# Kernel tuning notes

Hardware: AMD Instinct MI355X
Metric: run time of the kernel (lower is better)

## Reference

```python
import jax, jax.numpy as jnp
import numpy as np

B, S, H, NH, L, FF, V, T = 16, 256, 768, 12, 12, 3072, 30522, 9
DH = H // NH
LN_EPS = 1e-12


def _ln(x, g, b):
    m = jnp.mean(x, axis=-1, keepdims=True)
    v = jnp.mean((x - m) ** 2, axis=-1, keepdims=True)
    return (x - m) * jax.lax.rsqrt(v + LN_EPS) * g + b


def setup_inputs():
    key = jax.random.key(0)
    ks = jax.random.split(key, 20)
    n = lambda i, shape: jax.random.normal(ks[i], shape, jnp.float32) * 0.02
    lengths = jax.random.randint(ks[0], (B,), S // 2, S + 1)
    attention_mask = (jnp.arange(S)[None, :] < lengths[:, None]).astype(jnp.int32)
    return {
        "input_ids": jax.random.randint(ks[1], (B, S), 0, V),
        "attention_mask": attention_mask,
        "labels": jax.random.randint(ks[2], (B, S), 0, T),
        "word_emb": n(3, (V, H)),
        "pos_emb": n(4, (512, H)),
        "type_emb": n(5, (2, H)),
        "emb_g": jnp.ones((H,), jnp.float32), "emb_b": jnp.zeros((H,), jnp.float32),
        "lWq": n(6, (L, H, H)), "lbq": jnp.zeros((L, H), jnp.float32),
        "lWk": n(7, (L, H, H)), "lbk": jnp.zeros((L, H), jnp.float32),
        "lWv": n(8, (L, H, H)), "lbv": jnp.zeros((L, H), jnp.float32),
        "lWo": n(9, (L, H, H)), "lbo": jnp.zeros((L, H), jnp.float32),
        "lg1": jnp.ones((L, H), jnp.float32), "lb1": jnp.zeros((L, H), jnp.float32),
        "lWi": n(10, (L, H, FF)), "lbi": jnp.zeros((L, FF), jnp.float32),
        "lWf": n(11, (L, FF, H)), "lbf": jnp.zeros((L, H), jnp.float32),
        "lg2": jnp.ones((L, H), jnp.float32), "lb2": jnp.zeros((L, H), jnp.float32),
        "cls_W": n(12, (H, T)), "cls_b": jnp.zeros((T,), jnp.float32),
        "crf_start": jax.random.uniform(ks[13], (T,), jnp.float32, -0.1, 0.1),
        "crf_end": jax.random.uniform(ks[14], (T,), jnp.float32, -0.1, 0.1),
        "crf_trans": jax.random.uniform(ks[15], (T, T), jnp.float32, -0.1, 0.1),
    }


def _encoder(input_ids, attention_mask, word_emb, pos_emb, type_emb, emb_g, emb_b, layer_stack, cls_W, cls_b):
    x = word_emb[input_ids] + pos_emb[:S][None] + type_emb[0][None, None]  # [B,S,H]
    x = _ln(x, emb_g, emb_b)
    bias = (1.0 - attention_mask.astype(jnp.float32))[:, None, None, :] * -1e9  # [B,1,1,S]
    scale = 1.0 / np.sqrt(DH).astype(np.float32)

    def layer(h, p):
        Wq, bq, Wk, bk, Wv, bv, Wo, bo, g1, b1, Wi, bi, Wf, bf, g2, b2 = p
        q = (h @ Wq + bq).reshape(B, S, NH, DH)
        k = (h @ Wk + bk).reshape(B, S, NH, DH)
        v = (h @ Wv + bv).reshape(B, S, NH, DH)
        att = jax.nn.softmax(jnp.einsum('bqhd,bkhd->bhqk', q, k) * scale + bias, axis=-1)
        ctx = jnp.einsum('bhqk,bkhd->bqhd', att, v).reshape(B, S, H)
        h = _ln(h + ctx @ Wo + bo, g1, b1)
        ff = jax.nn.gelu(h @ Wi + bi, approximate=False) @ Wf + bf
        h = _ln(h + ff, g2, b2)
        return h, None

    x, _ = jax.lax.scan(layer, x, layer_stack)
    return x @ cls_W + cls_b  # [B,S,T]


def _crf_llh(em, tg, m, start, end, trans):
    # pytorch-crf forward, reduction='sum'. em [B,Lc,T], tg [B,Lc] int, m [B,Lc] bool
    mf = m.astype(em.dtype)
    em_sc = jnp.take_along_axis(em, tg[..., None], axis=-1)[..., 0]  # [B,Lc]
    tr_sc = trans[tg[:, :-1], tg[:, 1:]]                             # [B,Lc-1]
    num = start[tg[:, 0]] + em_sc[:, 0] + jnp.sum(mf[:, 1:] * (tr_sc + em_sc[:, 1:]), axis=1)
    seq_ends = jnp.sum(m.astype(jnp.int32), axis=1) - 1
    last_tag = jnp.take_along_axis(tg, seq_ends[:, None], axis=1)[:, 0]
    num = num + end[last_tag]

    def step(score, xs):
        em_t, m_t = xs
        nxt = jax.nn.logsumexp(score[:, :, None] + trans[None] + em_t[:, None, :], axis=1)
        return jnp.where(m_t[:, None], nxt, score), None

    score0 = start[None] + em[:, 0]
    score, _ = jax.lax.scan(step, score0, (em[:, 1:].transpose(1, 0, 2), m[:, 1:].transpose(1, 0)))
    den = jax.nn.logsumexp(score + end[None], axis=1)
    return jnp.sum(num - den)


def _viterbi(em, start, end, trans):
    # decode over the FULL sequence with all-ones mask (matches crf.decode(logits))
    def step(score, em_t):
        cand = score[:, :, None] + trans[None] + em_t[:, None, :]  # [B,T,T]
        return jnp.max(cand, axis=1), jnp.argmax(cand, axis=1)

    score0 = start[None] + em[:, 0]
    score, hist = jax.lax.scan(step, score0, em[:, 1:].transpose(1, 0, 2))  # hist [S-1,B,T]
    last = jnp.argmax(score + end[None], axis=1)  # [B]

    def back(tag, h):
        prev = jnp.take_along_axis(h, tag[:, None], axis=1)[:, 0]
        return prev, prev

    _, rev = jax.lax.scan(back, last, hist, reverse=True)  # rev[i] = tag at time i, i in [0,S-2]
    tags = jnp.concatenate([rev.transpose(1, 0), last[:, None]], axis=1)  # [B,S]
    return tags.astype(jnp.float32)


def reference(input_ids, attention_mask, labels, word_emb, pos_emb, type_emb, emb_g, emb_b,
              lWq, lbq, lWk, lbk, lWv, lbv, lWo, lbo, lg1, lb1, lWi, lbi, lWf, lbf, lg2, lb2,
              cls_W, cls_b, crf_start, crf_end, crf_trans):
    layer_stack = (lWq, lbq, lWk, lbk, lWv, lbv, lWo, lbo, lg1, lb1, lWi, lbi, lWf, lbf, lg2, lb2)
    logits = _encoder(input_ids, attention_mask, word_emb, pos_emb, type_emb, emb_g, emb_b, layer_stack, cls_W, cls_b)
    str_lens = jnp.sum(attention_mask, axis=-1)
    pos = jnp.arange(S)[None, :]
    mask = attention_mask.astype(bool) & (pos > 0) & (pos != (str_lens - 1)[:, None])
    tags_in = jnp.where(mask, labels, jnp.zeros_like(labels))
    loss = -_crf_llh(logits[:, 1:], tags_in[:, 1:], mask[:, 1:], crf_start, crf_end, crf_trans)
    tags = _viterbi(logits, crf_start, crf_end, crf_trans)
    return (loss, tags)
```

## Files before the change

### kernel.cpp

```cpp
#include <hip/hip_runtime.h>

#define B_ 16
#define S_ 256
#define H_ 768
#define NH_ 12
#define DH_ 64
#define L_ 12
#define FF_ 3072
#define T_ 9
#define NTOK (B_*S_)

#define AS1 __attribute__((address_space(1)))
#define AS3 __attribute__((address_space(3)))

typedef __attribute__((ext_vector_type(8))) short bfrag;
typedef __attribute__((ext_vector_type(8))) unsigned short us8;
typedef __attribute__((ext_vector_type(4))) float f4;

#define LOG2E_ 1.4426950408889634f
#define LN2_   0.6931471805599453f

__device__ inline unsigned short f2bf(float x) {
    unsigned u = __builtin_bit_cast(unsigned, x);
    return (unsigned short)((u + 0x7fffu + ((u >> 16) & 1u)) >> 16);
}
__device__ inline float bf2f(unsigned short h) {
    unsigned u = ((unsigned)h) << 16;
    return __builtin_bit_cast(float, u);
}
__device__ inline void pack8(const float* v, us8& h, us8& l) {
    #pragma unroll
    for (int j = 0; j < 8; j++) {
        unsigned short hh = f2bf(v[j]);
        h[j] = hh;
        l[j] = f2bf(v[j] - bf2f(hh));
    }
}

__global__ __launch_bounds__(256) void k_conv_w(
    const float* __restrict__ Wq, const float* __restrict__ Wk,
    const float* __restrict__ Wv, const float* __restrict__ Wo,
    const float* __restrict__ Wi, const float* __restrict__ Wf,
    const float* __restrict__ bq, const float* __restrict__ bk, const float* __restrict__ bv,
    float* __restrict__ qkvbias, unsigned short* __restrict__ Wpk)
{
    int bid = blockIdx.x;
    int tid = threadIdx.x;
    if (bid == 0) {
        for (int i = tid; i < 3 * H_; i += 256)
            qkvbias[i] = (i < H_) ? bq[i] : (i < 2 * H_) ? bk[i - H_] : bv[i - 2 * H_];
    }
    const float* src; int Kd, Nd; size_t doff; int t;
    if (bid < 576)       { int m = bid / 144; src = (m == 0) ? Wq : (m == 1) ? Wk : (m == 2) ? Wv : Wo;
                           Kd = H_; Nd = H_; doff = (size_t)m * 73728; t = bid % 144; }
    else if (bid < 1152) { src = Wi; Kd = H_; Nd = FF_; doff = 294912; t = bid - 576; }
    else                 { src = Wf; Kd = FF_; Nd = H_; doff = 589824; t = bid - 1152; }
    int ntn = Nd / 64;
    int tk = t / ntn, tn = t % ntn;
    int k0 = tk * 64, n0 = tn * 64;
    __shared__ float tile[64][65];
    int r = tid >> 6, c = tid & 63;
    #pragma unroll
    for (int i = 0; i < 16; i++)
        tile[r + i * 4][c] = src[(size_t)(k0 + r + i * 4) * Nd + n0 + c];
    __syncthreads();
    #pragma unroll
    for (int e = 0; e < 2; e++) {
        int item = tid * 2 + e;
        int nl = item >> 3, kb = item & 7;
        float v8[8];
        #pragma unroll
        for (int j = 0; j < 8; j++) v8[j] = tile[kb * 8 + j][nl];
        us8 h, l; pack8(v8, h, l);
        unsigned short* p = Wpk + (doff + (size_t)(n0 + nl) * (Kd / 8) + (k0 / 8 + kb)) * 16;
        *reinterpret_cast<us8*>(p) = h;
        *reinterpret_cast<us8*>(p + 8) = l;
    }
}

__global__ __launch_bounds__(128) void k_embed_ln(
    const int* __restrict__ ids, const float* __restrict__ wemb,
    const float* __restrict__ pemb, const float* __restrict__ temb,
    const float* __restrict__ g, const float* __restrict__ bb,
    float* __restrict__ out, unsigned short* __restrict__ out_pk)
{
    int tok = blockIdx.x;
    int s = tok & (S_ - 1);
    int id = ids[tok];
    int tid = threadIdx.x;
    bool act = tid < 96;
    int idx = tid * 8;
    float v8[8];
    float sum = 0.f;
    if (act) {
        const float4* w4 = reinterpret_cast<const float4*>(wemb + (size_t)id * H_ + idx);
        const float4* p4 = reinterpret_cast<const float4*>(pemb + (size_t)s * H_ + idx);
        const float4* t4 = reinterpret_cast<const float4*>(temb + idx);
        #pragma unroll
        for (int q = 0; q < 2; q++) {
            float4 a = w4[q], b = p4[q], c = t4[q];
            v8[q*4+0] = a.x + b.x + c.x; v8[q*4+1] = a.y + b.y + c.y;
            v8[q*4+2] = a.z + b.z + c.z; v8[q*4+3] = a.w + b.w + c.w;
        }
        #pragma unroll
        for (int j = 0; j < 8; j++) sum += v8[j];
    }
    __shared__ float wsum[2], wvar[2];
    #pragma unroll
    for (int o = 32; o > 0; o >>= 1) sum += __shfl_xor(sum, o);
    if ((tid & 63) == 0) wsum[tid >> 6] = sum;
    __syncthreads();
    float mean = (wsum[0] + wsum[1]) * (1.0f / H_);
    float vs = 0.f;
    if (act) {
        for (int j = 0; j < 8; j++) { float d = v8[j] - mean; vs += d * d; }
    }
    #pragma unroll
    for (int o = 32; o > 0; o >>= 1) vs += __shfl_xor(vs, o);
    if ((tid & 63) == 0) wvar[tid >> 6] = vs;
    __syncthreads();
    float inv = 1.0f / sqrtf((wvar[0] + wvar[1]) * (1.0f / H_) + 1e-12f);
    if (act) {
        float o8[8];
        #pragma unroll
        for (int j = 0; j < 8; j++) o8[j] = (v8[j] - mean) * inv * g[idx + j] + bb[idx + j];
        float4* d4 = reinterpret_cast<float4*>(out + (size_t)tok * H_ + idx);
        d4[0] = make_float4(o8[0], o8[1], o8[2], o8[3]);
        d4[1] = make_float4(o8[4], o8[5], o8[6], o8[7]);
        us8 h, l; pack8(o8, h, l);
        unsigned short* p = out_pk + ((size_t)tok * 96 + tid) * 16;
        *reinterpret_cast<us8*>(p) = h;
        *reinterpret_cast<us8*>(p + 8) = l;
    }
}

__global__ __launch_bounds__(128) void k_res_ln(
    const float* __restrict__ x, const float* __restrict__ res,
    const float* __restrict__ g, const float* __restrict__ bb,
    float* __restrict__ out, unsigned short* __restrict__ out_pk)
{
    int tok = blockIdx.x;
    int tid = threadIdx.x;
    bool act = tid < 96;
    int idx = tid * 8;
    float v8[8];
    float sum = 0.f;
    if (act) {
        const float4* x4 = reinterpret_cast<const float4*>(x + (size_t)tok * H_ + idx);
        const float4* r4 = reinterpret_cast<const float4*>(res + (size_t)tok * H_ + idx);
        #pragma unroll
        for (int q = 0; q < 2; q++) {
            float4 a = x4[q], b = r4[q];
            v8[q*4+0] = a.x + b.x; v8[q*4+1] = a.y + b.y;
            v8[q*4+2] = a.z + b.z; v8[q*4+3] = a.w + b.w;
        }
        #pragma unroll
        for (int j = 0; j < 8; j++) sum += v8[j];
    }
    __shared__ float wsum[2], wvar[2];
    #pragma unroll
    for (int o = 32; o > 0; o >>= 1) sum += __shfl_xor(sum, o);
    if ((tid & 63) == 0) wsum[tid >> 6] = sum;
    __syncthreads();
    float mean = (wsum[0] + wsum[1]) * (1.0f / H_);
    float vs = 0.f;
    if (act) {
        for (int j = 0; j < 8; j++) { float d = v8[j] - mean; vs += d * d; }
    }
    #pragma unroll
    for (int o = 32; o > 0; o >>= 1) vs += __shfl_xor(vs, o);
    if ((tid & 63) == 0) wvar[tid >> 6] = vs;
    __syncthreads();
    float inv = 1.0f / sqrtf((wvar[0] + wvar[1]) * (1.0f / H_) + 1e-12f);
    if (act) {
        float o8[8];
        #pragma unroll
        for (int j = 0; j < 8; j++) o8[j] = (v8[j] - mean) * inv * g[idx + j] + bb[idx + j];
        float4* d4 = reinterpret_cast<float4*>(out + (size_t)tok * H_ + idx);
        d4[0] = make_float4(o8[0], o8[1], o8[2], o8[3]);
        d4[1] = make_float4(o8[4], o8[5], o8[6], o8[7]);
        us8 h, l; pack8(o8, h, l);
        unsigned short* p = out_pk + ((size_t)tok * 96 + tid) * 16;
        *reinterpret_cast<us8*>(p) = h;
        *reinterpret_cast<us8*>(p + 8) = l;
    }
}

__global__ __launch_bounds__(256) void k_gemm_pk(
    const unsigned short* __restrict__ A, const unsigned short* __restrict__ Wp,
    const float* __restrict__ bias,
    float* __restrict__ C0, float* __restrict__ C1, float* __restrict__ C2, int cpb,
    unsigned short* __restrict__ Cpk,
    int M, int N, int K, int act, int cbx)
{
    constexpr int BUFSZ = 24576;
    __shared__ char smem[3 * BUFSZ];
    unsigned smb = (unsigned)(size_t)(void*)smem;

    int id = blockIdx.x;
    int xcd = id & 7;
    int rr = id >> 3;
    int by = (xcd >> 1) * 8 + rr / cbx;
    int bx = (xcd & 1) * cbx + rr % cbx;
    int m0 = by << 7, n0 = bx << 6;
    int Kb = K >> 3;
    int nst = Kb >> 2;
    int rowbytes = Kb * 32;

    int tid = threadIdx.x;
    int lane = tid & 63, wid = tid >> 6;
    int wm = wid >> 1, wn = wid & 1;
    int fr = lane & 15, fq = lane >> 4;

    f4 acc[4][2];
    #pragma unroll
    for (int i = 0; i < 4; i++)
        #pragma unroll
        for (int j = 0; j < 2; j++) acc[i][j] = (f4){0.f, 0.f, 0.f, 0.f};

    const char* agp[4];
    const char* bgp[2];
    #pragma unroll
    for (int i = 0; i < 4; i++) {
        int d = i * 4096 + tid * 16;
        int row = d >> 7;
        int colp = (d & 127) ^ ((row & 7) << 4);
        agp[i] = (const char*)A + (size_t)(m0 + row) * rowbytes + colp;
    }
    #pragma unroll
    for (int i = 0; i < 2; i++) {
        int d = i * 4096 + tid * 16;
        int row = d >> 7;
        int colp = (d & 127) ^ ((row & 7) << 4);
        bgp[i] = (const char*)Wp + (size_t)(n0 + row) * rowbytes + colp;
    }

    int afo[4], bfo[2];
    #pragma unroll
    for (int mi = 0; mi < 4; mi++) {
        int r = wm * 64 + mi * 16 + fr;
        afo[mi] = r * 128 + ((fq * 32) ^ ((r & 7) << 4));
    }
    #pragma unroll
    for (int ni = 0; ni < 2; ni++) {
        int rb = wn * 32 + ni * 16 + fr;
        bfo[ni] = 16384 + rb * 128 + ((fq * 32) ^ ((rb & 7) << 4));
    }

    auto issue = [&](int ks, unsigned boff) {
        size_t ko = (size_t)ks * 128;
        #pragma unroll
        for (int i = 0; i < 4; i++)
            __builtin_amdgcn_global_load_lds((const AS1 void*)(size_t)(agp[i] + ko),
                (AS3 void*)(unsigned)(smb + boff + i * 4096 + wid * 1024), 16, 0, 0);
        #pragma unroll
        for (int i = 0; i < 2; i++)
            __builtin_amdgcn_global_load_lds((const AS1 void*)(size_t)(bgp[i] + ko),
                (AS3 void*)(unsigned)(smb + boff + 16384 + i * 4096 + wid * 1024), 16, 0, 0);
    };

    issue(0, 0);
    if (nst > 1) issue(1, BUFSZ);
    unsigned c0 = 0, c1 = BUFSZ, c2 = 2 * BUFSZ;

    for (int ks = 0; ks < nst; ks++) {
        if (ks + 2 < nst) issue(ks + 2, c2);
        if (ks + 2 < nst)      asm volatile("s_waitcnt vmcnt(12)" ::: "memory");
        else if (ks + 1 < nst) asm volatile("s_waitcnt vmcnt(6)" ::: "memory");
        else                   asm volatile("s_waitcnt vmcnt(0)" ::: "memory");
        __builtin_amdgcn_s_barrier();
        __builtin_amdgcn_sched_barrier(0);

        const char* cbp = smem + c0;
        bfrag ah[4], al[4], bh[2], bl[2];
        #pragma unroll
        for (int mi = 0; mi < 4; mi++) {
            ah[mi] = *reinterpret_cast<const bfrag*>(cbp + afo[mi]);
            al[mi] = *reinterpret_cast<const bfrag*>(cbp + (afo[mi] ^ 16));
        }
        #pragma unroll
        for (int ni = 0; ni < 2; ni++) {
            bh[ni] = *reinterpret_cast<const bfrag*>(cbp + bfo[ni]);
            bl[ni] = *reinterpret_cast<const bfrag*>(cbp + (bfo[ni] ^ 16));
        }
        #pragma unroll
        for (int mi = 0; mi < 4; mi++) {
            #pragma unroll
            for (int ni = 0; ni < 2; ni++) {
                acc[mi][ni] = __builtin_amdgcn_mfma_f32_16x16x32_bf16(ah[mi], bh[ni], acc[mi][ni], 0, 0, 0);
                acc[mi][ni] = __builtin_amdgcn_mfma_f32_16x16x32_bf16(ah[mi], bl[ni], acc[mi][ni], 0, 0, 0);
                acc[mi][ni] = __builtin_amdgcn_mfma_f32_16x16x32_bf16(al[mi], bh[ni], acc[mi][ni], 0, 0, 0);
            }
        }
        __builtin_amdgcn_s_barrier();
        __builtin_amdgcn_sched_barrier(0);
        unsigned t = c0; c0 = c1; c1 = c2; c2 = t;
    }

    if (act == 0) {
        #pragma unroll
        for (int mi = 0; mi < 4; mi++) {
            #pragma unroll
            for (int ni = 0; ni < 2; ni++) {
                int col = n0 + wn * 32 + ni * 16 + fr;
                float bv = bias[col];
                int buf = col / cpb;
                float* Cp = (buf == 0) ? C0 : (buf == 1) ? C1 : C2;
                int cc = col - buf * cpb;
                #pragma unroll
                for (int r = 0; r < 4; r++) {
                    int row = m0 + wm * 64 + mi * 16 + fq * 4 + r;
                    Cp[(size_t)row * cpb + cc] = acc[mi][ni][r] + bv;
                }
            }
        }
    } else {
        float* ebuf = (float*)(smem + wid * 2432);
        int Nb = N >> 3;
        #pragma unroll
        for (int mi = 0; mi < 4; mi++) {
            #pragma unroll
            for (int ni = 0; ni < 2; ni++) {
                int col = n0 + wn * 32 + ni * 16 + fr;
                float bv = bias[col];
                #pragma unroll
                for (int r = 0; r < 4; r++) {
                    float v = acc[mi][ni][r] + bv;
                    v = 0.5f * v * (1.0f + erff(v * 0.70710678118654752f));
                    ebuf[(fq * 4 + r) * 38 + ni * 16 + fr] = v;
                }
            }
            int row16 = lane >> 2, kb = lane & 3;
            float v8[8];
            #pragma unroll
            for (int j = 0; j < 8; j++) v8[j] = ebuf[row16 * 38 + kb * 8 + j];
            us8 h, l; pack8(v8, h, l);
            int grow = m0 + wm * 64 + mi * 16 + row16;
            int gcb = ((n0 + wn * 32) >> 3) + kb;
            unsigned short* p = Cpk + ((size_t)grow * Nb + gcb) * 16;
            *reinterpret_cast<us8*>(p) = h;
            *reinterpret_cast<us8*>(p + 8) = l;
        }
    }
}

#define SM_KH 0
#define SM_KL 5632
#define SM_VH 11264
#define SM_VL 16384
#define SM_PH 21504
#define SM_PL 26624
__global__ __launch_bounds__(256) void k_attn_fused(
    const float* __restrict__ Q, const float* __restrict__ Kb,
    const float* __restrict__ V, const int* __restrict__ amask,
    unsigned short* __restrict__ ctx_pk)
{
    __shared__ char smem[31744];
    unsigned short* KhS = (unsigned short*)(smem + SM_KH);
    unsigned short* KlS = (unsigned short*)(smem + SM_KL);
    unsigned short* VhS = (unsigned short*)(smem + SM_VH);
    unsigned short* VlS = (unsigned short*)(smem + SM_VL);
    unsigned short* PhS = (unsigned short*)(smem + SM_PH);
    unsigned short* PlS = (unsigned short*)(smem + SM_PL);

    int idx = blockIdx.x;
    int qt = idx & 3;
    int hd = (idx >> 2) % NH_;
    int b = idx / (4 * NH_);
    int tid = threadIdx.x;
    int lane = tid & 63, wid = tid >> 6;
    int fr = lane & 15, fq = lane >> 4;

    int q0 = qt * 64 + wid * 16;

    bfrag qh[2], ql[2];
    {
        const float* qbase = Q + ((size_t)(b * S_ + q0 + fr)) * H_ + hd * DH_;
        #pragma unroll
        for (int ks = 0; ks < 2; ks++) {
            const float4* p = reinterpret_cast<const float4*>(qbase + ks * 32 + fq * 8);
            float4 v0 = p[0], v1 = p[1];
            float vv[8] = {v0.x, v0.y, v0.z, v0.w, v1.x, v1.y, v1.z, v1.w};
            #pragma unroll
            for (int j = 0; j < 8; j++) {
                unsigned short h = f2bf(vv[j]);
                qh[ks][j] = (short)h;
                ql[ks][j] = (short)f2bf(vv[j] - bf2f(h));
            }
        }
    }

    f4 o[4];
    #pragma unroll
    for (int i = 0; i < 4; i++) o[i] = (f4){0.f, 0.f, 0.f, 0.f};
    float m[4], l[4];
    #pragma unroll
    for (int r = 0; r < 4; r++) { m[r] = -3e38f; l[r] = 0.f; }

    int kvrow = tid >> 3;
    int dbase = (tid & 7) * 8;

    for (int t = 0; t < 8; t++) {
        {
            const float* src = Kb + ((size_t)(b * S_ + t * 32 + kvrow)) * H_ + hd * DH_ + dbase;
            float4 a4 = reinterpret_cast<const float4*>(src)[0];
            float4 b4 = reinterpret_cast<const float4*>(src)[1];
            float vv[8] = {a4.x, a4.y, a4.z, a4.w, b4.x, b4.y, b4.z, b4.w};
            us8 h, l2;
            #pragma unroll
            for (int j = 0; j < 8; j++) {
                unsigned short hh = f2bf(vv[j]);
                h[j] = hh; l2[j] = f2bf(vv[j] - bf2f(hh));
            }
            *reinterpret_cast<us8*>(&KhS[kvrow * 88 + dbase]) = h;
            *reinterpret_cast<us8*>(&KlS[kvrow * 88 + dbase]) = l2;
        }
        {
            const float* src = V + ((size_t)(b * S_ + t * 32 + kvrow)) * H_ + hd * DH_ + dbase;
            float4 a4 = reinterpret_cast<const float4*>(src)[0];
            float4 b4 = reinterpret_cast<const float4*>(src)[1];
            float vv[8] = {a4.x, a4.y, a4.z, a4.w, b4.x, b4.y, b4.z, b4.w};
            #pragma unroll
            for (int j = 0; j < 8; j++) {
                unsigned short h = f2bf(vv[j]);
                VhS[(dbase + j) * 40 + kvrow] = h;
                VlS[(dbase + j) * 40 + kvrow] = f2bf(vv[j] - bf2f(h));
            }
        }
        __syncthreads();

        f4 s0 = (f4){0.f,0.f,0.f,0.f}, s1 = (f4){0.f,0.f,0.f,0.f};
        #pragma unroll
        for (int ks = 0; ks < 2; ks++) {
            bfrag kbh0 = *reinterpret_cast<const bfrag*>(&KhS[fr * 88 + ks * 32 + fq * 8]);
            bfrag kbl0 = *reinterpret_cast<const bfrag*>(&KlS[fr * 88 + ks * 32 + fq * 8]);
            bfrag kbh1 = *reinterpret_cast<const bfrag*>(&KhS[(16 + fr) * 88 + ks * 32 + fq * 8]);
            bfrag kbl1 = *reinterpret_cast<const bfrag*>(&KlS[(16 + fr) * 88 + ks * 32 + fq * 8]);
            s0 = __builtin_amdgcn_mfma_f32_16x16x32_bf16(qh[ks], kbh0, s0, 0, 0, 0);
            s0 = __builtin_amdgcn_mfma_f32_16x16x32_bf16(qh[ks], kbl0, s0, 0, 0, 0);
            s0 = __builtin_amdgcn_mfma_f32_16x16x32_bf16(ql[ks], kbh0, s0, 0, 0, 0);
            s1 = __builtin_amdgcn_mfma_f32_16x16x32_bf16(qh[ks], kbh1, s1, 0, 0, 0);
            s1 = __builtin_amdgcn_mfma_f32_16x16x32_bf16(qh[ks], kbl1, s1, 0, 0, 0);
            s1 = __builtin_amdgcn_mfma_f32_16x16x32_bf16(ql[ks], kbh1, s1, 0, 0, 0);
        }

        float cb0 = (amask[b * S_ + t * 32 + fr] == 0) ? -1e9f : 0.f;
        float cb1 = (amask[b * S_ + t * 32 + 16 + fr] == 0) ? -1e9f : 0.f;
        float sc0[4], sc1[4], fct[4], pr0[4], pr1[4];
        #pragma unroll
        for (int r = 0; r < 4; r++) {
            sc0[r] = s0[r] * 0.125f + cb0;
            sc1[r] = s1[r] * 0.125f + cb1;
            float tm = fmaxf(sc0[r], sc1[r]);
            #pragma unroll
            for (int od = 1; od < 16; od <<= 1) tm = fmaxf(tm, __shfl_xor(tm, od));
            float mn = fmaxf(m[r], tm);
            fct[r] = expf(m[r] - mn);
            pr0[r] = expf(sc0[r] - mn);
            pr1[r] = expf(sc1[r] - mn);
            float rs = pr0[r] + pr1[r];
            #pragma unroll
            for (int od = 1; od < 16; od <<= 1) rs += __shfl_xor(rs, od);
            l[r] = l[r] * fct[r] + rs;
            m[r] = mn;
        }
        #pragma unroll
        for (int ci = 0; ci < 4; ci++)
            #pragma unroll
            for (int r = 0; r < 4; r++) o[ci][r] *= fct[r];

        #pragma unroll
        for (int r = 0; r < 4; r++) {
            int row = fq * 4 + r;
            unsigned short h0 = f2bf(pr0[r]);
            PhS[wid * 640 + row * 40 + fr] = h0;
            PlS[wid * 640 + row * 40 + fr] = f2bf(pr0[r] - bf2f(h0));
            unsigned short h1 = f2bf(pr1[r]);
            PhS[wid * 640 + row * 40 + 16 + fr] = h1;
            PlS[wid * 640 + row * 40 + 16 + fr] = f2bf(pr1[r] - bf2f(h1));
        }

        bfrag pah = *reinterpret_cast<const bfrag*>(&PhS[wid * 640 + fr * 40 + fq * 8]);
        bfrag pal = *reinterpret_cast<const bfrag*>(&PlS[wid * 640 + fr * 40 + fq * 8]);
        #pragma unroll
        for (int ci = 0; ci < 4; ci++) {
            bfrag vbh = *reinterpret_cast<const bfrag*>(&VhS[(ci * 16 + fr) * 40 + fq * 8]);
            bfrag vbl = *reinterpret_cast<const bfrag*>(&VlS[(ci * 16 + fr) * 40 + fq * 8]);
            o[ci] = __builtin_amdgcn_mfma_f32_16x16x32_bf16(pah, vbh, o[ci], 0, 0, 0);
            o[ci] = __builtin_amdgcn_mfma_f32_16x16x32_bf16(pah, vbl, o[ci], 0, 0, 0);
            o[ci] = __builtin_amdgcn_mfma_f32_16x16x32_bf16(pal, vbh, o[ci], 0, 0, 0);
        }
        __syncthreads();
    }

    __syncthreads();
    float* eb = (float*)smem + wid * 1088;
    #pragma unroll
    for (int r = 0; r < 4; r++) {
        float inv = 1.0f / l[r];
        #pragma unroll
        for (int ci = 0; ci < 4; ci++)
            eb[(fq * 4 + r) * 68 + ci * 16 + fr] = o[ci][r] * inv;
    }
    __syncthreads();
    #pragma unroll
    for (int e = 0; e < 2; e++) {
        int item = lane * 2 + e;
        int row16 = item >> 3, kb = item & 7;
        float v8[8];
        #pragma unroll
        for (int j = 0; j < 8; j++) v8[j] = eb[row16 * 68 + kb * 8 + j];
        us8 h, l2; pack8(v8, h, l2);
        int grow = b * S_ + q0 + row16;
        int gcb = hd * 8 + kb;
        unsigned short* p = ctx_pk + ((size_t)grow * 96 + gcb) * 16;
        *reinterpret_cast<us8*>(p) = h;
        *reinterpret_cast<us8*>(p + 8) = l2;
    }
}

__global__ __launch_bounds__(64) void k_classifier(
    const float* __restrict__ Hs, const float* __restrict__ Wc,
    const float* __restrict__ bc, float* __restrict__ logits)
{
    int tok = blockIdx.x;
    int lane = threadIdx.x;
    const float* hr = Hs + (size_t)tok * H_;
    float acc[T_];
    #pragma unroll
    for (int j = 0; j < T_; j++) acc[j] = 0.f;
    for (int k = lane; k < H_; k += 64) {
        float hv = hr[k];
        const float* wr = Wc + (size_t)k * T_;
        #pragma unroll
        for (int j = 0; j < T_; j++) acc[j] = fmaf(hv, wr[j], acc[j]);
    }
    #pragma unroll
    for (int j = 0; j < T_; j++) {
        float v = acc[j];
        for (int o = 32; o > 0; o >>= 1) v += __shfl_down(v, o);
        if (lane == 0) logits[(size_t)tok * T_ + j] = v + bc[j];
    }
}

__global__ __launch_bounds__(256) void k_crf_vit(
    const float* __restrict__ logits, const int* __restrict__ amask,
    const int* __restrict__ labels, const float* __restrict__ start,
    const float* __restrict__ endv, const float* __restrict__ trans,
    float* __restrict__ out)
{
    int blk = blockIdx.x;
    int tid = threadIdx.x;
    if (blk == 0) {
        __shared__ float res[B_];
        int lane = tid & 63;
        int bb = (tid >> 6) * 4 + (lane >> 4);
        int sj = lane & 15;
        int lb = lane & 48;

        int cnt = 0;
        for (int s = sj; s < S_; s += 16) cnt += amask[bb * S_ + s];
        #pragma unroll
        for (int o = 8; o > 0; o >>= 1) cnt += __shfl_xor(cnt, o);
        int len = cnt;
        int lim = len - 1;

        float num = 0.f;
        for (int s = 2 + sj; s < S_; s += 16) {
            if (s < lim) {
                int tp = labels[bb * S_ + s - 1];
                int tc = labels[bb * S_ + s];
                num += trans[tp * T_ + tc] + logits[((size_t)(bb * S_ + s)) * T_ + tc];
            }
        }
        #pragma unroll
        for (int o = 8; o > 0; o >>= 1) num += __shfl_xor(num, o);
        int tg1 = labels[bb * S_ + 1];
        num += start[tg1] + logits[((size_t)(bb * S_ + 1)) * T_ + tg1];
        num += endv[labels[bb * S_ + (len - 2)]];

        float tc9[T_];
        #pragma unroll
        for (int i = 0; i < T_; i++) tc9[i] = (sj < T_) ? trans[i * T_ + sj] * LOG2E_ : 0.f;
        float score = (sj < T_) ? (start[sj] + logits[((size_t)(bb * S_ + 1)) * T_ + sj]) * LOG2E_ : 0.f;
        const float* embase = logits + (size_t)bb * S_ * T_ + sj;
        float emb[8];
        #pragma unroll
        for (int c = 0; c < 8; c++) emb[c] = (sj < T_) ? embase[(2 + c) * T_] : 0.f;
        for (int s0 = 2; s0 < S_; s0 += 8) {
            #pragma unroll
            for (int c = 0; c < 8; c++) {
                int s = s0 + c;
                if (s < S_) {
                    float em = emb[c];
                    emb[c] = (sj < T_ && s + 8 < S_) ? embase[(size_t)(s + 8) * T_] : 0.f;
                    float si[T_];
                    #pragma unroll
                    for (int i = 0; i < T_; i++) si[i] = __shfl(score, lb + i);
                    float a9[T_];
                    #pragma unroll
                    for (int i = 0; i < T_; i++) a9[i] = si[i] + tc9[i];
                    float mx = a9[0];
                    #pragma unroll
                    for (int i = 1; i < T_; i++) mx = fmaxf(mx, a9[i]);
                    float sum = 0.f;
                    #pragma unroll
                    for (int i = 0; i < T_; i++) sum += exp2f(a9[i] - mx);
                    float nsc = fmaf(em, LOG2E_, mx + log2f(sum));
                    if (s < lim) score = nsc;
                }
            }
        }
        float se = (sj < T_) ? score + endv[sj] * LOG2E_ : -1e30f;
        float fi[T_];
        #pragma unroll
        for (int i = 0; i < T_; i++) fi[i] = __shfl(se, lb + i);
        if (sj == 0) {
            float mx = -1e30f;
            #pragma unroll
            for (int i = 0; i < T_; i++) mx = fmaxf(mx, fi[i]);
            float sum = 0.f;
            #pragma unroll
            for (int i = 0; i < T_; i++) sum += exp2f(fi[i] - mx);
            res[bb] = (mx + log2f(sum)) * LN2_ - num;
        }
        __syncthreads();
        if (tid == 0) {
            float tot = 0.f;
            #pragma unroll
            for (int i = 0; i < B_; i++) tot += res[i];
            out[0] = tot;
        }
    } else {
        if (tid >= 64) return;
        int b = blk - 1;
        int j = tid;
        float* tags_out = out + 1;
        __shared__ unsigned char hist[S_ - 1][T_];
        float tc9[T_];
        #pragma unroll
        for (int i = 0; i < T_; i++) tc9[i] = (j < T_) ? trans[i * T_ + j] : 0.f;
        float score = (j < T_) ? start[j] + logits[((size_t)(b * S_)) * T_ + j] : -1e30f;
        const float* embase = logits + (size_t)b * S_ * T_ + j;
        float emb[8];
        #pragma unroll
        for (int c = 0; c < 8; c++) emb[c] = (j < T_) ? embase[(1 + c) * T_] : 0.f;
        for (int t0 = 1; t0 < S_; t0 += 8) {
            #pragma unroll
            for (int c = 0; c < 8; c++) {
                int t = t0 + c;
                if (t < S_) {
                    float em = emb[c];
                    emb[c] = (j < T_ && t + 8 < S_) ? embase[(size_t)(t + 8) * T_] : 0.f;
                    float si[T_];
                    #pragma unroll
                    for (int i = 0; i < T_; i++) si[i] = __shfl(score, i);
                    float best = -1e30f; int bi = 0;
                    #pragma unroll
                    for (int i = 0; i < T_; i++) {
                        float cv = si[i] + tc9[i];
                        if (cv > best) { best = cv; bi = i; }
                    }
                    if (j < T_) {
                        hist[t - 1][j] = (unsigned char)bi;
                        score = best + em;
                    }
                }
            }
        }
        float se = (j < T_) ? score + endv[j] : -1e30f;
        float fi[T_];
        #pragma unroll
        for (int i = 0; i < T_; i++) fi[i] = __shfl(se, i);
        if (j == 0) {
            float best = -1e30f; int last = 0;
            #pragma unroll
            for (int i = 0; i < T_; i++) if (fi[i] > best) { best = fi[i]; last = i; }
            tags_out[b * S_ + (S_ - 1)] = (float)last;
            int cur = last;
            for (int t = S_ - 2; t >= 0; t--) {
                cur = hist[t][cur];
                tags_out[b * S_ + t] = (float)cur;
            }
        }
    }
}

extern "C" void kernel_launch(void* const* d_in, const int* in_sizes, int n_in,
                              void* d_out, int out_size, void* d_ws, size_t ws_size,
                              hipStream_t stream)
{
    const int*   input_ids = (const int*)d_in[0];
    const int*   amask     = (const int*)d_in[1];
    const int*   labels    = (const int*)d_in[2];
    const float* word_emb  = (const float*)d_in[3];
    const float* pos_emb   = (const float*)d_in[4];
    const float* type_emb  = (const float*)d_in[5];
    const float* emb_g     = (const float*)d_in[6];
    const float* emb_b     = (const float*)d_in[7];
    const float* lWq = (const float*)d_in[8];
    const float* lbq = (const float*)d_in[9];
    const float* lWk = (const float*)d_in[10];
    const float* lbk = (const float*)d_in[11];
    const float* lWv = (const float*)d_in[12];
    const float* lbv = (const float*)d_in[13];
    const float* lWo = (const float*)d_in[14];
    const float* lbo = (const float*)d_in[15];
    const float* lg1 = (const float*)d_in[16];
    const float* lb1 = (const float*)d_in[17];
    const float* lWi = (const float*)d_in[18];
    const float* lbi = (const float*)d_in[19];
    const float* lWf = (const float*)d_in[20];
    const float* lbf = (const float*)d_in[21];
    const float* lg2 = (const float*)d_in[22];
    const float* lb2 = (const float*)d_in[23];
    const float* cls_W = (const float*)d_in[24];
    const float* cls_b = (const float*)d_in[25];
    const float* crf_start = (const float*)d_in[26];
    const float* crf_end   = (const float*)d_in[27];
    const float* crf_trans = (const float*)d_in[28];

    float* out = (float*)d_out;
    float* ws = (float*)d_ws;

    const size_t NH32 = (size_t)NTOK * H_;
    float* h       = ws;
    float* h_pk_f  = ws + NH32;
    float* q       = ws + 2 * NH32;
    float* kbuf    = ws + 3 * NH32;
    float* v       = ws + 4 * NH32;
    float* ctxpk_f = ws + 5 * NH32;
    float* tmp     = ws + 6 * NH32;
    float* Wpk_f   = ws + 7 * NH32;
    float* qkvbias = Wpk_f + 7077888;
    float* logits  = qkvbias + 3 * H_;

    unsigned short* h_pk   = (unsigned short*)h_pk_f;
    unsigned short* ctx_pk = (unsigned short*)ctxpk_f;
    unsigned short* Wpk    = (unsigned short*)Wpk_f;
    unsigned short* big_pk = (unsigned short*)q;

    k_embed_ln<<<NTOK, 128, 0, stream>>>(input_ids, word_emb, pos_emb, type_emb, emb_g, emb_b, h, h_pk);

    const size_t WOFF_O = 221184, WOFF_I = 294912, WOFF_F = 589824;

    for (int l = 0; l < L_; l++) {
        k_conv_w<<<1728, 256, 0, stream>>>(
            lWq + (size_t)l * H_ * H_, lWk + (size_t)l * H_ * H_,
            lWv + (size_t)l * H_ * H_, lWo + (size_t)l * H_ * H_,
            lWi + (size_t)l * H_ * FF_, lWf + (size_t)l * FF_ * H_,
            lbq + (size_t)l * H_, lbk + (size_t)l * H_, lbv + (size_t)l * H_,
            qkvbias, Wpk);

        k_gemm_pk<<<1152, 256, 0, stream>>>(h_pk, Wpk, qkvbias,
            q, kbuf, v, H_, nullptr, NTOK, 3 * H_, H_, 0, 18);

        k_attn_fused<<<B_ * NH_ * 4, 256, 0, stream>>>(q, kbuf, v, amask, ctx_pk);

        k_gemm_pk<<<384, 256, 0, stream>>>(ctx_pk, Wpk + WOFF_O * 16, lbo + (size_t)l * H_,
            tmp, tmp, tmp, H_, nullptr, NTOK, H_, H_, 0, 6);

        k_res_ln<<<NTOK, 128, 0, stream>>>(tmp, h, lg1 + (size_t)l * H_, lb1 + (size_t)l * H_, h, h_pk);

        k_gemm_pk<<<1536, 256, 0, stream>>>(h_pk, Wpk + WOFF_I * 16, lbi + (size_t)l * FF_,
            tmp, tmp, tmp, FF_, big_pk, NTOK, FF_, H_, 1, 24);

        k_gemm_pk<<<384, 256, 0, stream>>>(big_pk, Wpk + WOFF_F * 16, lbf + (size_t)l * H_,
            tmp, tmp, tmp, H_, nullptr, NTOK, H_, FF_, 0, 6);

        k_res_ln<<<NTOK, 128, 0, stream>>>(tmp, h, lg2 + (size_t)l * H_, lb2 + (size_t)l * H_, h, h_pk);
    }

    k_classifier<<<NTOK, 64, 0, stream>>>(h, cls_W, cls_b, logits);
    k_crf_vit<<<1 + B_, 256, 0, stream>>>(logits, amask, labels, crf_start, crf_end, crf_trans, out);
}
```

Measured before the change: 3.608 ms.

## Drop fp32 hidden copy, reorder GEMM prefetch barrier, simplify CRF reductions

The fp32 hidden-state buffer is removed. Residual adds and the classifier now rebuild activations from the packed bf16 hi/lo pair, which cuts global traffic in the LayerNorm and classifier kernels. The GEMM main loop issues the next-stage prefetch after the barrier and drops the second per-iteration barrier, adding a syncthreads before the epilogue. The CRF forward pass swaps max-subtraction for periodic rebasing of the score, and Viterbi uses a tree argmax. These changes risk small precision differences, and the triple-buffer ordering may race if the buffer reuse distance is off.

```diff
diff --git a/kernel.cpp b/kernel.cpp
--- a/kernel.cpp
+++ b/kernel.cpp
@@ -82,7 +82,7 @@
     const int* __restrict__ ids, const float* __restrict__ wemb,
     const float* __restrict__ pemb, const float* __restrict__ temb,
     const float* __restrict__ g, const float* __restrict__ bb,
-    float* __restrict__ out, unsigned short* __restrict__ out_pk)
+    unsigned short* __restrict__ out_pk)
 {
     int tok = blockIdx.x;
     int s = tok & (S_ - 1);
@@ -124,9 +124,6 @@
         float o8[8];
         #pragma unroll
         for (int j = 0; j < 8; j++) o8[j] = (v8[j] - mean) * inv * g[idx + j] + bb[idx + j];
-        float4* d4 = reinterpret_cast<float4*>(out + (size_t)tok * H_ + idx);
-        d4[0] = make_float4(o8[0], o8[1], o8[2], o8[3]);
-        d4[1] = make_float4(o8[4], o8[5], o8[6], o8[7]);
         us8 h, l; pack8(o8, h, l);
         unsigned short* p = out_pk + ((size_t)tok * 96 + tid) * 16;
         *reinterpret_cast<us8*>(p) = h;
@@ -135,9 +132,8 @@
 }
 
 __global__ __launch_bounds__(128) void k_res_ln(
-    const float* __restrict__ x, const float* __restrict__ res,
-    const float* __restrict__ g, const float* __restrict__ bb,
-    float* __restrict__ out, unsigned short* __restrict__ out_pk)
+    const float* __restrict__ x, const float* __restrict__ g, const float* __restrict__ bb,
+    unsigned short* __restrict__ h_pk)
 {
     int tok = blockIdx.x;
     int tid = threadIdx.x;
@@ -145,17 +141,18 @@
     int idx = tid * 8;
     float v8[8];
     float sum = 0.f;
+    unsigned short* p = h_pk + ((size_t)tok * 96 + tid) * 16;
     if (act) {
         const float4* x4 = reinterpret_cast<const float4*>(x + (size_t)tok * H_ + idx);
-        const float4* r4 = reinterpret_cast<const float4*>(res + (size_t)tok * H_ + idx);
-        #pragma unroll
-        for (int q = 0; q < 2; q++) {
-            float4 a = x4[q], b = r4[q];
-            v8[q*4+0] = a.x + b.x; v8[q*4+1] = a.y + b.y;
-            v8[q*4+2] = a.z + b.z; v8[q*4+3] = a.w + b.w;
-        }
-        #pragma unroll
-        for (int j = 0; j < 8; j++) sum += v8[j];
+        us8 hi = *reinterpret_cast<const us8*>(p);
+        us8 lo = *reinterpret_cast<const us8*>(p + 8);
+        float4 a0 = x4[0], a1 = x4[1];
+        float xs[8] = {a0.x, a0.y, a0.z, a0.w, a1.x, a1.y, a1.z, a1.w};
+        #pragma unroll
+        for (int j = 0; j < 8; j++) {
+            v8[j] = xs[j] + bf2f(hi[j]) + bf2f(lo[j]);
+            sum += v8[j];
+        }
     }
     __shared__ float wsum[2], wvar[2];
     #pragma unroll
@@ -176,11 +173,7 @@
         float o8[8];
         #pragma unroll
         for (int j = 0; j < 8; j++) o8[j] = (v8[j] - mean) * inv * g[idx + j] + bb[idx + j];
-        float4* d4 = reinterpret_cast<float4*>(out + (size_t)tok * H_ + idx);
-        d4[0] = make_float4(o8[0], o8[1], o8[2], o8[3]);
-        d4[1] = make_float4(o8[4], o8[5], o8[6], o8[7]);
         us8 h, l; pack8(o8, h, l);
-        unsigned short* p = out_pk + ((size_t)tok * 96 + tid) * 16;
         *reinterpret_cast<us8*>(p) = h;
         *reinterpret_cast<us8*>(p + 8) = l;
     }
@@ -264,12 +257,11 @@
     unsigned c0 = 0, c1 = BUFSZ, c2 = 2 * BUFSZ;
 
     for (int ks = 0; ks < nst; ks++) {
-        if (ks + 2 < nst) issue(ks + 2, c2);
-        if (ks + 2 < nst)      asm volatile("s_waitcnt vmcnt(12)" ::: "memory");
-        else if (ks + 1 < nst) asm volatile("s_waitcnt vmcnt(6)" ::: "memory");
-        else                   asm volatile("s_waitcnt vmcnt(0)" ::: "memory");
+        if (ks + 1 < nst) asm volatile("s_waitcnt vmcnt(6)" ::: "memory");
+        else              asm volatile("s_waitcnt vmcnt(0)" ::: "memory");
         __builtin_amdgcn_s_barrier();
         __builtin_amdgcn_sched_barrier(0);
+        if (ks + 2 < nst) issue(ks + 2, c2);
 
         const char* cbp = smem + c0;
         bfrag ah[4], al[4], bh[2], bl[2];
@@ -292,8 +284,6 @@
                 acc[mi][ni] = __builtin_amdgcn_mfma_f32_16x16x32_bf16(al[mi], bh[ni], acc[mi][ni], 0, 0, 0);
             }
         }
-        __builtin_amdgcn_s_barrier();
-        __builtin_amdgcn_sched_barrier(0);
         unsigned t = c0; c0 = c1; c1 = c2; c2 = t;
     }
 
@@ -315,6 +305,7 @@
             }
         }
     } else {
+        __syncthreads();
         float* ebuf = (float*)(smem + wid * 2432);
         int Nb = N >> 3;
         #pragma unroll
@@ -520,20 +511,25 @@
 }
 
 __global__ __launch_bounds__(64) void k_classifier(
-    const float* __restrict__ Hs, const float* __restrict__ Wc,
+    const unsigned short* __restrict__ Hpk, const float* __restrict__ Wc,
     const float* __restrict__ bc, float* __restrict__ logits)
 {
     int tok = blockIdx.x;
     int lane = threadIdx.x;
-    const float* hr = Hs + (size_t)tok * H_;
     float acc[T_];
     #pragma unroll
     for (int j = 0; j < T_; j++) acc[j] = 0.f;
-    for (int k = lane; k < H_; k += 64) {
-        float hv = hr[k];
-        const float* wr = Wc + (size_t)k * T_;
-        #pragma unroll
-        for (int j = 0; j < T_; j++) acc[j] = fmaf(hv, wr[j], acc[j]);
+    for (int kb = lane; kb < 96; kb += 64) {
+        const unsigned short* p = Hpk + ((size_t)tok * 96 + kb) * 16;
+        us8 hi = *reinterpret_cast<const us8*>(p);
+        us8 lo = *reinterpret_cast<const us8*>(p + 8);
+        #pragma unroll
+        for (int e = 0; e < 8; e++) {
+            float hv = bf2f(hi[e]) + bf2f(lo[e]);
+            const float* wr = Wc + (size_t)(kb * 8 + e) * T_;
+            #pragma unroll
+            for (int j = 0; j < T_; j++) acc[j] = fmaf(hv, wr[j], acc[j]);
+        }
     }
     #pragma unroll
     for (int j = 0; j < T_; j++) {
@@ -583,6 +579,7 @@
         #pragma unroll
         for (int i = 0; i < T_; i++) tc9[i] = (sj < T_) ? trans[i * T_ + sj] * LOG2E_ : 0.f;
         float score = (sj < T_) ? (start[sj] + logits[((size_t)(bb * S_ + 1)) * T_ + sj]) * LOG2E_ : 0.f;
+        float base = 0.f;
         const float* embase = logits + (size_t)bb * S_ * T_ + sj;
         float emb[8];
         #pragma unroll
@@ -597,19 +594,19 @@
                     float si[T_];
                     #pragma unroll
                     for (int i = 0; i < T_; i++) si[i] = __shfl(score, lb + i);
-                    float a9[T_];
+                    float e2[T_];
                     #pragma unroll
-                    for (int i = 0; i < T_; i++) a9[i] = si[i] + tc9[i];
-                    float mx = a9[0];
-                    #pragma unroll
-                    for (int i = 1; i < T_; i++) mx = fmaxf(mx, a9[i]);
-                    float sum = 0.f;
-                    #pragma unroll
-                    for (int i = 0; i < T_; i++) sum += exp2f(a9[i] - mx);
-                    float nsc = fmaf(em, LOG2E_, mx + log2f(sum));
+                    for (int i = 0; i < T_; i++) e2[i] = exp2f(si[i] + tc9[i]);
+                    float s01 = e2[0] + e2[1], s23 = e2[2] + e2[3];
+                    float s45 = e2[4] + e2[5], s67 = e2[6] + e2[7];
+                    float sum = ((s01 + s23) + (s45 + s67)) + e2[8];
+                    float nsc = fmaf(em, LOG2E_, log2f(sum));
                     if (s < lim) score = nsc;
                 }
             }
+            float sh = __shfl(score, lb);
+            score -= sh;
+            base += sh;
         }
         float se = (sj < T_) ? score + endv[sj] * LOG2E_ : -1e30f;
         float fi[T_];
@@ -622,7 +619,7 @@
             float sum = 0.f;
             #pragma unroll
             for (int i = 0; i < T_; i++) sum += exp2f(fi[i] - mx);
-            res[bb] = (mx + log2f(sum)) * LN2_ - num;
+            res[bb] = (base + mx + log2f(sum)) * LN2_ - num;
         }
         __syncthreads();
         if (tid == 0) {
@@ -655,12 +652,17 @@
                     float si[T_];
                     #pragma unroll
                     for (int i = 0; i < T_; i++) si[i] = __shfl(score, i);
-                    float best = -1e30f; int bi = 0;
+                    float cv[T_];
                     #pragma unroll
-                    for (int i = 0; i < T_; i++) {
-                        float cv = si[i] + tc9[i];
-                        if (cv > best) { best = cv; bi = i; }
-                    }
+                    for (int i = 0; i < T_; i++) cv[i] = si[i] + tc9[i];
+                    float v01 = cv[0]; int i01 = 0; if (cv[1] > v01) { v01 = cv[1]; i01 = 1; }
+                    float v23 = cv[2]; int i23 = 2; if (cv[3] > v23) { v23 = cv[3]; i23 = 3; }
+                    float v45 = cv[4]; int i45 = 4; if (cv[5] > v45) { v45 = cv[5]; i45 = 5; }
+                    float v67 = cv[6]; int i67 = 6; if (cv[7] > v67) { v67 = cv[7]; i67 = 7; }
+                    float v03 = v01; int i03 = i01; if (v23 > v03) { v03 = v23; i03 = i23; }
+                    float v47 = v45; int i47 = i45; if (v67 > v47) { v47 = v67; i47 = i67; }
+                    float v07 = v03; int i07 = i03; if (v47 > v07) { v07 = v47; i07 = i47; }
+                    float best = v07; int bi = i07; if (cv[8] > best) { best = cv[8]; bi = 8; }
                     if (j < T_) {
                         hist[t - 1][j] = (unsigned char)bi;
                         score = best + em;
@@ -724,7 +726,6 @@
     float* ws = (float*)d_ws;
 
     const size_t NH32 = (size_t)NTOK * H_;
-    float* h       = ws;
     float* h_pk_f  = ws + NH32;
     float* q       = ws + 2 * NH32;
     float* kbuf    = ws + 3 * NH32;
@@ -740,7 +741,7 @@
     unsigned short* Wpk    = (unsigned short*)Wpk_f;
     unsigned short* big_pk = (unsigned short*)q;
 
-    k_embed_ln<<<NTOK, 128, 0, stream>>>(input_ids, word_emb, pos_emb, type_emb, emb_g, emb_b, h, h_pk);
+    k_embed_ln<<<NTOK, 128, 0, stream>>>(input_ids, word_emb, pos_emb, type_emb, emb_g, emb_b, h_pk);
 
     const size_t WOFF_O = 221184, WOFF_I = 294912, WOFF_F = 589824;
 
@@ -760,7 +761,7 @@
         k_gemm_pk<<<384, 256, 0, stream>>>(ctx_pk, Wpk + WOFF_O * 16, lbo + (size_t)l * H_,
             tmp, tmp, tmp, H_, nullptr, NTOK, H_, H_, 0, 6);
 
-        k_res_ln<<<NTOK, 128, 0, stream>>>(tmp, h, lg1 + (size_t)l * H_, lb1 + (size_t)l * H_, h, h_pk);
+        k_res_ln<<<NTOK, 128, 0, stream>>>(tmp, lg1 + (size_t)l * H_, lb1 + (size_t)l * H_, h_pk);
 
         k_gemm_pk<<<1536, 256, 0, stream>>>(h_pk, Wpk + WOFF_I * 16, lbi + (size_t)l * FF_,
             tmp, tmp, tmp, FF_, big_pk, NTOK, FF_, H_, 1, 24);
@@ -768,9 +769,9 @@
         k_gemm_pk<<<384, 256, 0, stream>>>(big_pk, Wpk + WOFF_F * 16, lbf + (size_t)l * H_,
             tmp, tmp, tmp, H_, nullptr, NTOK, H_, FF_, 0, 6);
 
-        k_res_ln<<<NTOK, 128, 0, stream>>>(tmp, h, lg2 + (size_t)l * H_, lb2 + (size_t)l * H_, h, h_pk);
-    }
-
-    k_classifier<<<NTOK, 64, 0, stream>>>(h, cls_W, cls_b, logits);
+        k_res_ln<<<NTOK, 128, 0, stream>>>(tmp, lg2 + (size_t)l * H_, lb2 + (size_t)l * H_, h_pk);
+    }
+
+    k_classifier<<<NTOK, 64, 0, stream>>>(h_pk, cls_W, cls_b, logits);
     k_crf_vit<<<1 + B_, 256, 0, stream>>>(logits, amask, labels, crf_start, crf_end, crf_trans, out);
 }
```

Result: no change. 3.570 ms (median of 2 runs) (-1.1%).
